# Kernel tuning notes

Measured on AMD Instinct MI355X. Metric: run time of the kernel, lower is better.

The kernel has to match this reference:

```python
import jax, jax.numpy as jnp
import numpy as np

T, B, DIM, D_INNER, N_STATE = 2048, 8, 1024, 2048, 64


def setup_inputs() -> dict:
    key = jax.random.key(0)
    ks = jax.random.split(key, 7)

    def w(k, shape, fan_in):
        return jax.random.normal(k, shape, jnp.float32) / np.float32(np.sqrt(fan_in))

    return {
        "x": jax.random.normal(ks[0], (T, B, DIM), jnp.float32),
        "W_in": w(ks[1], (D_INNER, DIM), DIM),      # in_proj (torch Linear weight layout)
        "W_k": w(ks[2], (N_STATE, D_INNER), D_INNER),
        "W_v": w(ks[3], (N_STATE, D_INNER), D_INNER),
        "W_q": w(ks[4], (N_STATE, D_INNER), D_INNER),
        "W_z": w(ks[5], (N_STATE, D_INNER), D_INNER),  # output-gate projection
        "W_out": w(ks[6], (DIM, N_STATE), N_STATE),  # out_proj
    }


def _forward(x, W_in, W_k, W_v, W_q, W_z, W_out):
    # x: [T, B, dim] -> h: [T, B, d_inner]
    h = jnp.einsum('tbd,id->tbi', x, W_in)
    # per-token cell projections: [T, B, n_state]
    k = jnp.einsum('tbi,ni->tbn', h, W_k)
    k = k / (jnp.linalg.norm(k, axis=-1, keepdims=True) + 1e-6)  # unit-norm key (stable delta rule)
    v = jnp.einsum('tbi,ni->tbn', h, W_v)
    q = jnp.einsum('tbi,ni->tbn', h, W_q)
    z = jnp.einsum('tbi,ni->tbn', h, W_z)

    S0 = jnp.zeros((x.shape[1], N_STATE, N_STATE), x.dtype)  # full-matrix state per batch

    def step(S, kvqz):
        kt, vt, qt, zt = kvqz                              # each [B, n_state]
        pred = jnp.einsum('bnm,bm->bn', S, kt)
        S = S + jnp.einsum('bn,bm->bnm', vt - pred, kt)    # delta-rule update
        y = jnp.tanh(jnp.einsum('bnm,bm->bn', S, qt)) * jax.nn.sigmoid(zt)  # tanh readout + output gate
        return S, y

    _, ys = jax.lax.scan(step, S0, (k, v, q, z))           # ys: [T, B, n_state]
    return jnp.einsum('tbn,dn->tbd', ys, W_out)            # out_proj -> [T, B, dim]


def reference(x, W_in, W_k, W_v, W_q, W_z, W_out):
    return _forward(x, W_in, W_k, W_v, W_q, W_z, W_out)
```

## Files before the change

kernel.cpp:

```cpp
#include <hip/hip_runtime.h>
#include <math.h>

#define TT   2048
#define BB   8
#define DIM_ 1024
#define DI_  2048
#define NS_  64
#define MR_  (TT * BB)
#define NCH  32
#define LD   68
#define KSPL 16
#define KCH  (DI_ / KSPL)
#define NGRP 8
#define GSZ  4
#define LDH2 40

typedef _Float16 half8 __attribute__((ext_vector_type(8)));
typedef _Float16 half4h __attribute__((ext_vector_type(4)));
typedef float floatx4 __attribute__((ext_vector_type(4)));

__device__ __forceinline__ float dot4(float4 a, float4 b) {
  return a.x * b.x + a.y * b.y + a.z * b.z + a.w * b.w;
}

__device__ __forceinline__ half8 cvt8(float4 lo, float4 hi) {
  half8 h = {(_Float16)lo.x, (_Float16)lo.y, (_Float16)lo.z, (_Float16)lo.w,
             (_Float16)hi.x, (_Float16)hi.y, (_Float16)hi.z, (_Float16)hi.w};
  return h;
}

__global__ __launch_bounds__(256) void cvt_f16_kernel(
    const float* __restrict__ in, _Float16* __restrict__ out, long n8) {
  long i = (long)blockIdx.x * 256 + threadIdx.x;
  const long stride = (long)gridDim.x * 256;
  for (; i < n8; i += stride) {
    const float4 lo = *(const float4*)&in[i * 8];
    const float4 hi = *(const float4*)&in[i * 8 + 4];
    *(half8*)&out[i * 8] = cvt8(lo, hi);
  }
}

__global__ __launch_bounds__(256) void gemm_h16(
    const _Float16* __restrict__ A, const _Float16* __restrict__ B,
    float* __restrict__ C, int M, int N, int K) {
  __shared__ __align__(16) _Float16 Ah[2][64 * LDH2];
  __shared__ __align__(16) _Float16 Bh[2][64 * LDH2];
  const int tid  = threadIdx.x;
  const int m0   = blockIdx.y * 64;
  const int n0   = blockIdx.x * 64;
  const int wave = tid >> 6, lane = tid & 63;
  const int wm   = (wave >> 1) * 32;
  const int wn   = (wave & 1) * 32;
  const int quad = lane >> 4, l16 = lane & 15;
  const int srow = tid >> 2;
  const int scol = (tid & 3) * 8;

  const _Float16* Ap = A + (size_t)(m0 + srow) * K + scol;
  const _Float16* Bp = B + (size_t)(n0 + srow) * K + scol;

  floatx4 acc[2][2];
#pragma unroll
  for (int i = 0; i < 2; ++i)
#pragma unroll
    for (int j = 0; j < 2; ++j) acc[i][j] = (floatx4)0.f;

  half8 ha, hb;
  ha = *(const half8*)(Ap);
  hb = *(const half8*)(Bp);
  *(half8*)&Ah[0][srow * LDH2 + scol] = ha;
  *(half8*)&Bh[0][srow * LDH2 + scol] = hb;
  __syncthreads();

  const int NK = K >> 5;
  for (int kt = 0; kt < NK; ++kt) {
    const int cur = kt & 1;
    if (kt + 1 < NK) {
      ha = *(const half8*)(Ap + (kt + 1) * 32);
      hb = *(const half8*)(Bp + (kt + 1) * 32);
    }
    half8 af[2], bf[2];
#pragma unroll
    for (int mt = 0; mt < 2; ++mt)
      af[mt] = *(const half8*)&Ah[cur][(wm + mt * 16 + l16) * LDH2 + quad * 8];
#pragma unroll
    for (int nt = 0; nt < 2; ++nt)
      bf[nt] = *(const half8*)&Bh[cur][(wn + nt * 16 + l16) * LDH2 + quad * 8];
#pragma unroll
    for (int mt = 0; mt < 2; ++mt)
#pragma unroll
      for (int nt = 0; nt < 2; ++nt)
        acc[mt][nt] = __builtin_amdgcn_mfma_f32_16x16x32_f16(
            af[mt], bf[nt], acc[mt][nt], 0, 0, 0);
    if (kt + 1 < NK) {
      const int nxt = cur ^ 1;
      *(half8*)&Ah[nxt][srow * LDH2 + scol] = ha;
      *(half8*)&Bh[nxt][srow * LDH2 + scol] = hb;
    }
    __syncthreads();
  }

#pragma unroll
  for (int mt = 0; mt < 2; ++mt) {
#pragma unroll
    for (int i = 0; i < 4; ++i) {
      const size_t r = (size_t)(m0 + wm + mt * 16 + quad * 4 + i) * N;
#pragma unroll
      for (int nt = 0; nt < 2; ++nt)
        C[r + n0 + wn + nt * 16 + l16] = acc[mt][nt][i];
    }
  }
}

__global__ __launch_bounds__(256) void fuse_gemm_kernel(
    const float* __restrict__ Wk, const float* __restrict__ Wv,
    const float* __restrict__ Wq, const float* __restrict__ Wz,
    const float* __restrict__ Win, float* __restrict__ Pg) {
  __shared__ __align__(16) float As[16][132];
  __shared__ __align__(16) float Bs[16][132];
  const int tid = threadIdx.x;
  const int n0  = blockIdx.x * 128;
  const int m0  = blockIdx.y * 128;
  const int kb  = blockIdx.z * KCH;
  const int lrow = tid >> 2;
  const int lk4  = (tid & 3) << 2;
  const int tm   = (tid & 15) << 2;
  const int tn   = (tid >> 4) << 2;
  const float* Wg[4] = {Wk, Wv, Wq, Wz};
  const int ra = m0 + lrow, rb = m0 + 64 + lrow;
  const float* arow0 = Wg[ra >> 6] + (size_t)(ra & 63) * DI_;
  const float* arow1 = Wg[rb >> 6] + (size_t)(rb & 63) * DI_;
  const int brow = tid >> 5;
  const int bcol = (tid & 31) << 2;

  float acc[8][8];
#pragma unroll
  for (int i = 0; i < 8; ++i)
#pragma unroll
    for (int j = 0; j < 8; ++j) acc[i][j] = 0.f;

  for (int k0 = 0; k0 < KCH; k0 += 16) {
    float4 av0 = *(const float4*)&arow0[kb + k0 + lk4];
    float4 av1 = *(const float4*)&arow1[kb + k0 + lk4];
    float4 bv0 = *(const float4*)&Win[(size_t)(kb + k0 + brow)     * DIM_ + n0 + bcol];
    float4 bv1 = *(const float4*)&Win[(size_t)(kb + k0 + 8 + brow) * DIM_ + n0 + bcol];
    __syncthreads();
    As[lk4 + 0][lrow] = av0.x; As[lk4 + 1][lrow] = av0.y;
    As[lk4 + 2][lrow] = av0.z; As[lk4 + 3][lrow] = av0.w;
    As[lk4 + 0][64 + lrow] = av1.x; As[lk4 + 1][64 + lrow] = av1.y;
    As[lk4 + 2][64 + lrow] = av1.z; As[lk4 + 3][64 + lrow] = av1.w;
    *(float4*)&Bs[brow][bcol]     = bv0;
    *(float4*)&Bs[brow + 8][bcol] = bv1;
    __syncthreads();
#pragma unroll
    for (int kk = 0; kk < 16; ++kk) {
      float4 a0 = *(const float4*)&As[kk][tm];
      float4 a1 = *(const float4*)&As[kk][tm + 64];
      float4 b0 = *(const float4*)&Bs[kk][tn];
      float4 b1 = *(const float4*)&Bs[kk][tn + 64];
      float ar[8] = {a0.x, a0.y, a0.z, a0.w, a1.x, a1.y, a1.z, a1.w};
      float br[8] = {b0.x, b0.y, b0.z, b0.w, b1.x, b1.y, b1.z, b1.w};
#pragma unroll
      for (int i = 0; i < 8; ++i)
#pragma unroll
        for (int j = 0; j < 8; ++j)
          acc[i][j] = fmaf(ar[i], br[j], acc[i][j]);
    }
  }
  float* P = Pg + (size_t)blockIdx.z * (256 * DIM_);
#pragma unroll
  for (int i = 0; i < 8; ++i) {
    int r = m0 + tm + (i & 3) + ((i >> 2) << 6);
    float4 c0 = make_float4(acc[i][0], acc[i][1], acc[i][2], acc[i][3]);
    float4 c1 = make_float4(acc[i][4], acc[i][5], acc[i][6], acc[i][7]);
    *(float4*)&P[(size_t)r * DIM_ + n0 + tn]      = c0;
    *(float4*)&P[(size_t)r * DIM_ + n0 + tn + 64] = c1;
  }
}

__global__ __launch_bounds__(256) void fuse_reduce_kernel(
    const float* __restrict__ Pg, _Float16* __restrict__ Wfh) {
  const size_t i = ((size_t)blockIdx.x * 256 + threadIdx.x) << 2;
  float4 s = *(const float4*)&Pg[i];
#pragma unroll
  for (int ks = 1; ks < KSPL; ++ks) {
    float4 p = *(const float4*)&Pg[(size_t)ks * (256 * DIM_) + i];
    s.x += p.x; s.y += p.y; s.z += p.z; s.w += p.w;
  }
  half4h h = {(_Float16)s.x, (_Float16)s.y, (_Float16)s.z, (_Float16)s.w};
  *(half4h*)&Wfh[i] = h;
}

__global__ __launch_bounds__(256) void norm_k_kernel(float* __restrict__ kvqz) {
  const int wid  = (blockIdx.x * 256 + threadIdx.x) >> 6;
  const int lane = threadIdx.x & 63;
  float x = kvqz[(size_t)wid * 256 + lane];
  float s = x * x;
  s += __shfl_xor(s, 1);  s += __shfl_xor(s, 2);  s += __shfl_xor(s, 4);
  s += __shfl_xor(s, 8);  s += __shfl_xor(s, 16); s += __shfl_xor(s, 32);
  kvqz[(size_t)wid * 256 + lane] = x / (sqrtf(s) + 1e-6f);
}

__global__ __launch_bounds__(256) void phase1_kernel(
    const float* __restrict__ kvqz, float* __restrict__ Tg,
    float* __restrict__ Mg, float* __restrict__ Bg) {
  __shared__ __align__(16) float Ks[64][LD];
  __shared__ __align__(16) float Vs[64][LD];
  __shared__ __align__(16) float As[64][LD];
  __shared__ __align__(16) float Tt[64][LD];
  const int cb = blockIdx.x;
  const int c  = cb >> 3, b = cb & 7;
  const int t  = threadIdx.x;

  {
    const int tau = t >> 2, m0 = (t & 3) << 4;
    const float* src = kvqz + (size_t)((c * 64 + tau) * BB + b) * 256;
#pragma unroll
    for (int u = 0; u < 4; ++u) {
      *(float4*)&Ks[tau][m0 + 4 * u] = *(const float4*)&src[m0 + 4 * u];
      *(float4*)&Vs[tau][m0 + 4 * u] = *(const float4*)&src[64 + m0 + 4 * u];
    }
  }
  __syncthreads();

  const int i0 = (t >> 4) << 2;
  const int j0 = (t & 15) << 2;

  {
    float acc[4][4];
#pragma unroll
    for (int i = 0; i < 4; ++i)
#pragma unroll
      for (int j = 0; j < 4; ++j) acc[i][j] = 0.f;
#pragma unroll 2
    for (int m4 = 0; m4 < 64; m4 += 4) {
      float4 ar[4], br[4];
#pragma unroll
      for (int i = 0; i < 4; ++i) ar[i] = *(const float4*)&Ks[i0 + i][m4];
#pragma unroll
      for (int j = 0; j < 4; ++j) br[j] = *(const float4*)&Ks[j0 + j][m4];
#pragma unroll
      for (int i = 0; i < 4; ++i)
#pragma unroll
        for (int j = 0; j < 4; ++j) acc[i][j] += dot4(ar[i], br[j]);
    }
#pragma unroll
    for (int i = 0; i < 4; ++i)
      *(float4*)&As[i0 + i][j0] =
          make_float4(acc[i][0], acc[i][1], acc[i][2], acc[i][3]);
  }
  __syncthreads();

  if (t < 64) {
    const int j = t;
    float tt[64];
    tt[0] = (j == 0) ? 1.f : 0.f;
#pragma unroll
    for (int i = 1; i < 64; ++i) {
      float p0 = 0.f, p1 = 0.f, p2 = 0.f, p3 = 0.f;
      const int nf = i >> 2;
#pragma unroll
      for (int s4 = 0; s4 < nf; ++s4) {
        float4 av = *(const float4*)&As[i][4 * s4];
        p0 = fmaf(av.x, tt[4 * s4 + 0], p0);
        p1 = fmaf(av.y, tt[4 * s4 + 1], p1);
        p2 = fmaf(av.z, tt[4 * s4 + 2], p2);
        p3 = fmaf(av.w, tt[4 * s4 + 3], p3);
      }
#pragma unroll
      for (int s = 4 * nf; s < i; ++s) p0 = fmaf(As[i][s], tt[s], p0);
      tt[i] = (i == j) ? 1.f : -((p0 + p1) + (p2 + p3));
    }
#pragma unroll
    for (int u = 0; u < 16; ++u)
      *(float4*)&Tt[j][4 * u] = make_float4(tt[4 * u + 0], tt[4 * u + 1],
                                            tt[4 * u + 2], tt[4 * u + 3]);
  }
  __syncthreads();

  {
    float accP[4][4], accV[4][4];
#pragma unroll
    for (int i = 0; i < 4; ++i)
#pragma unroll
      for (int j = 0; j < 4; ++j) { accP[i][j] = 0.f; accV[i][j] = 0.f; }
#pragma unroll 4
    for (int s = 0; s < 64; ++s) {
      float4 tv = *(const float4*)&Tt[s][i0];
      float4 kv = *(const float4*)&Ks[s][j0];
      float4 vv = *(const float4*)&Vs[s][j0];
      float ta[4] = {tv.x, tv.y, tv.z, tv.w};
      float ka[4] = {kv.x, kv.y, kv.z, kv.w};
      float va[4] = {vv.x, vv.y, vv.z, vv.w};
#pragma unroll
      for (int i = 0; i < 4; ++i)
#pragma unroll
        for (int j = 0; j < 4; ++j) {
          accP[i][j] = fmaf(ta[i], ka[j], accP[i][j]);
          accV[i][j] = fmaf(ta[i], va[j], accV[i][j]);
        }
    }
    __syncthreads();
#pragma unroll
    for (int i = 0; i < 4; ++i) {
      *(float4*)&As[i0 + i][j0] =
          make_float4(accP[i][0], accP[i][1], accP[i][2], accP[i][3]);
      *(float4*)&Vs[i0 + i][j0] =
          make_float4(accV[i][0], accV[i][1], accV[i][2], accV[i][3]);
    }
  }
  __syncthreads();

  {
    float accM[4][4], accB[4][4];
#pragma unroll
    for (int i = 0; i < 4; ++i)
#pragma unroll
      for (int j = 0; j < 4; ++j) { accM[i][j] = 0.f; accB[i][j] = 0.f; }
#pragma unroll 4
    for (int s = 0; s < 64; ++s) {
      float4 pv  = *(const float4*)&As[s][i0];
      float4 pvv = *(const float4*)&Vs[s][i0];
      float4 kv  = *(const float4*)&Ks[s][j0];
      float pa[4] = {pv.x, pv.y, pv.z, pv.w};
      float qa[4] = {pvv.x, pvv.y, pvv.z, pvv.w};
      float ka[4] = {kv.x, kv.y, kv.z, kv.w};
#pragma unroll
      for (int i = 0; i < 4; ++i)
#pragma unroll
        for (int j = 0; j < 4; ++j) {
          accM[i][j] = fmaf(pa[i], ka[j], accM[i][j]);
          accB[i][j] = fmaf(qa[i], ka[j], accB[i][j]);
        }
    }
    const size_t base = (size_t)cb * 4096;
#pragma unroll
    for (int i = 0; i < 4; ++i) {
      float m0v = ((i0 + i) == (j0 + 0)) ? 1.f : 0.f;
      float m1v = ((i0 + i) == (j0 + 1)) ? 1.f : 0.f;
      float m2v = ((i0 + i) == (j0 + 2)) ? 1.f : 0.f;
      float m3v = ((i0 + i) == (j0 + 3)) ? 1.f : 0.f;
      *(float4*)&Mg[base + (size_t)(i0 + i) * 64 + j0] =
          make_float4(m0v - accM[i][0], m1v - accM[i][1],
                      m2v - accM[i][2], m3v - accM[i][3]);
      *(float4*)&Bg[base + (size_t)(i0 + i) * 64 + j0] =
          make_float4(accB[i][0], accB[i][1], accB[i][2], accB[i][3]);
    }
    const int fr = t >> 2, fc = (t & 3) << 4;
#pragma unroll
    for (int u = 0; u < 4; ++u)
      *(float4*)&Tg[base + (size_t)fr * 64 + fc + 4 * u] =
          *(const float4*)&Tt[fr][fc + 4 * u];
  }
}

__global__ __launch_bounds__(64, 1) void p2a_kernel(
    const float* __restrict__ Mg, const float* __restrict__ Bg,
    float* __restrict__ Mcum, float* __restrict__ Sall,
    float* __restrict__ BGfin) {
  __shared__ __align__(16) float Srow[2][4 * LD];
  const int bid  = blockIdx.x;
  const int g    = bid >> 8;
  const int b    = (bid >> 5) & 7;
  const int w    = bid & 31;
  const int lane = threadIdx.x;
  const int rr   = lane >> 4;
  const int jc   = lane & 15;
  const bool isB = (w >= 16);
  const int n    = ((w & 15) << 2) + rr;

  float4 cs;
  if (isB) cs = make_float4(0.f, 0.f, 0.f, 0.f);
  else
    cs = make_float4((jc * 4 + 0) == n ? 1.f : 0.f,
                     (jc * 4 + 1) == n ? 1.f : 0.f,
                     (jc * 4 + 2) == n ? 1.f : 0.f,
                     (jc * 4 + 3) == n ? 1.f : 0.f);

  for (int l = 0; l < GSZ; ++l) {
    const int c   = g * GSZ + l;
    const int cur = l & 1;
    const size_t cbase = ((size_t)c * BB + b) * 4096;
    if (isB) *(float4*)&Sall[cbase + (size_t)n * 64 + jc * 4] = cs;
    else if (l > 0) *(float4*)&Mcum[cbase + (size_t)n * 64 + jc * 4] = cs;
    *(float4*)&Srow[cur][rr * LD + jc * 4] = cs;
    float4 bv = make_float4(0.f, 0.f, 0.f, 0.f);
    if (isB) bv = *(const float4*)&Bg[cbase + (size_t)n * 64 + jc * 4];

    const float* Mrow = Mg + cbase + jc * 4;
    float4 acc = make_float4(0.f, 0.f, 0.f, 0.f);
#pragma unroll
    for (int u = 0; u < 16; ++u) {
      float4 sv = *(const float4*)&Srow[cur][rr * LD + u * 4];
      float4 m0 = *(const float4*)&Mrow[(4 * u + 0) * 64];
      float4 m1 = *(const float4*)&Mrow[(4 * u + 1) * 64];
      float4 m2 = *(const float4*)&Mrow[(4 * u + 2) * 64];
      float4 m3 = *(const float4*)&Mrow[(4 * u + 3) * 64];
      acc.x = fmaf(sv.x, m0.x, acc.x); acc.y = fmaf(sv.x, m0.y, acc.y);
      acc.z = fmaf(sv.x, m0.z, acc.z); acc.w = fmaf(sv.x, m0.w, acc.w);
      acc.x = fmaf(sv.y, m1.x, acc.x); acc.y = fmaf(sv.y, m1.y, acc.y);
      acc.z = fmaf(sv.y, m1.z, acc.z); acc.w = fmaf(sv.y, m1.w, acc.w);
      acc.x = fmaf(sv.z, m2.x, acc.x); acc.y = fmaf(sv.z, m2.y, acc.y);
      acc.z = fmaf(sv.z, m2.z, acc.z); acc.w = fmaf(sv.z, m2.w, acc.w);
      acc.x = fmaf(sv.w, m3.x, acc.x); acc.y = fmaf(sv.w, m3.y, acc.y);
      acc.z = fmaf(sv.w, m3.z, acc.z); acc.w = fmaf(sv.w, m3.w, acc.w);
    }
    cs = make_float4(acc.x + bv.x, acc.y + bv.y, acc.z + bv.z, acc.w + bv.w);
  }
  if (isB)
    *(float4*)&BGfin[((size_t)g * BB + b) * 4096 + (size_t)n * 64 + jc * 4] = cs;
  else
    *(float4*)&Mcum[((size_t)(g * GSZ) * BB + b) * 4096 + (size_t)n * 64 + jc * 4] = cs;
}

__global__ __launch_bounds__(64, 1) void p2b_kernel(
    const float* __restrict__ Mcum, const float* __restrict__ BGfin,
    float* __restrict__ Sall) {
  __shared__ __align__(16) float Srow[2][4 * LD];
  const int bid  = blockIdx.x;
  const int b    = bid >> 4;
  const int w    = bid & 15;
  const int lane = threadIdx.x;
  const int rr   = lane >> 4;
  const int jc   = lane & 15;
  const int n    = w * 4 + rr;

  float4 cs = make_float4(0.f, 0.f, 0.f, 0.f);

  for (int g2 = 0; g2 < NGRP - 1; ++g2) {
    const int cur = g2 & 1;
    *(float4*)&Srow[cur][rr * LD + jc * 4] = cs;
    float4 bv = *(const float4*)&BGfin[((size_t)g2 * BB + b) * 4096 +
                                       (size_t)n * 64 + jc * 4];
    const float* Mrow =
        Mcum + ((size_t)(g2 * GSZ) * BB + b) * 4096 + jc * 4;
    float4 acc = make_float4(0.f, 0.f, 0.f, 0.f);
#pragma unroll
    for (int u = 0; u < 16; ++u) {
      float4 sv = *(const float4*)&Srow[cur][rr * LD + u * 4];
      float4 m0 = *(const float4*)&Mrow[(4 * u + 0) * 64];
      float4 m1 = *(const float4*)&Mrow[(4 * u + 1) * 64];
      float4 m2 = *(const float4*)&Mrow[(4 * u + 2) * 64];
      float4 m3 = *(const float4*)&Mrow[(4 * u + 3) * 64];
      acc.x = fmaf(sv.x, m0.x, acc.x); acc.y = fmaf(sv.x, m0.y, acc.y);
      acc.z = fmaf(sv.x, m0.z, acc.z); acc.w = fmaf(sv.x, m0.w, acc.w);
      acc.x = fmaf(sv.y, m1.x, acc.x); acc.y = fmaf(sv.y, m1.y, acc.y);
      acc.z = fmaf(sv.y, m1.z, acc.z); acc.w = fmaf(sv.y, m1.w, acc.w);
      acc.x = fmaf(sv.z, m2.x, acc.x); acc.y = fmaf(sv.z, m2.y, acc.y);
      acc.z = fmaf(sv.z, m2.z, acc.z); acc.w = fmaf(sv.z, m2.w, acc.w);
      acc.x = fmaf(sv.w, m3.x, acc.x); acc.y = fmaf(sv.w, m3.y, acc.y);
      acc.z = fmaf(sv.w, m3.z, acc.z); acc.w = fmaf(sv.w, m3.w, acc.w);
    }
    cs = make_float4(acc.x + bv.x, acc.y + bv.y, acc.z + bv.z, acc.w + bv.w);
    *(float4*)&Sall[((size_t)((g2 + 1) * GSZ) * BB + b) * 4096 +
                    (size_t)n * 64 + jc * 4] = cs;
  }
}

__global__ __launch_bounds__(256) void p2c_kernel(
    const float* __restrict__ Mcum, float* __restrict__ Sall) {
  __shared__ __align__(16) float SgT[64][LD];
  __shared__ __align__(16) float Mc[64][LD];
  const int idx = blockIdx.x;
  const int b   = idx & 7;
  const int q   = idx >> 3;
  const int g   = 1 + q / (GSZ - 1);
  const int l   = 1 + q % (GSZ - 1);
  const int c   = g * GSZ + l;
  const int t   = threadIdx.x;
  const size_t cbase = ((size_t)c * BB + b) * 4096;
  const size_t gbase = ((size_t)(g * GSZ) * BB + b) * 4096;
  {
    const int tau = t & 63, c0 = (t >> 6) << 4;
    const float* sgp = Sall + gbase + (size_t)tau * 64 + c0;
    const float* mcp = Mcum + cbase + (size_t)tau * 64 + c0;
#pragma unroll
    for (int u = 0; u < 4; ++u) {
      float4 sv = *(const float4*)&sgp[4 * u];
      SgT[c0 + 4 * u + 0][tau] = sv.x;
      SgT[c0 + 4 * u + 1][tau] = sv.y;
      SgT[c0 + 4 * u + 2][tau] = sv.z;
      SgT[c0 + 4 * u + 3][tau] = sv.w;
      *(float4*)&Mc[tau][c0 + 4 * u] = *(const float4*)&mcp[4 * u];
    }
  }
  __syncthreads();
  const int i0 = (t >> 4) << 2;
  const int j0 = (t & 15) << 2;
  float acc[4][4];
#pragma unroll
  for (int i = 0; i < 4; ++i)
#pragma unroll
    for (int j = 0; j < 4; ++j) acc[i][j] = 0.f;
  for (int m = 0; m < 64; ++m) {
    float4 tv = *(const float4*)&SgT[m][i0];
    float4 kv = *(const float4*)&Mc[m][j0];
    float ta[4] = {tv.x, tv.y, tv.z, tv.w};
    float ka[4] = {kv.x, kv.y, kv.z, kv.w};
#pragma unroll
    for (int i = 0; i < 4; ++i)
#pragma unroll
      for (int j = 0; j < 4; ++j) acc[i][j] = fmaf(ta[i], ka[j], acc[i][j]);
  }
  float* dst = Sall + cbase;
#pragma unroll
  for (int i = 0; i < 4; ++i) {
    float4 d = *(float4*)&dst[(size_t)(i0 + i) * 64 + j0];
    d.x += acc[i][0]; d.y += acc[i][1];
    d.z += acc[i][2]; d.w += acc[i][3];
    *(float4*)&dst[(size_t)(i0 + i) * 64 + j0] = d;
  }
}

__global__ __launch_bounds__(256) void phase3_kernel(
    const float* __restrict__ kvqz, const float* __restrict__ Tg,
    const float* __restrict__ Sall, _Float16* __restrict__ ys) {
  __shared__ __align__(16) float Ks[64][LD];
  __shared__ __align__(16) float Qs[64][LD];
  __shared__ __align__(16) float S0s[64][LD];
  __shared__ __align__(16) float Gts[64][LD];
  const int cb = blockIdx.x;
  const int c  = cb >> 3, b = cb & 7;
  const int t  = threadIdx.x;
  const size_t base = (size_t)cb * 4096;

  {
    const int tau = t >> 2, m0 = (t & 3) << 4;
    const float* src = kvqz + (size_t)((c * 64 + tau) * BB + b) * 256;
#pragma unroll
    for (int u = 0; u < 4; ++u) {
      *(float4*)&Ks[tau][m0 + 4 * u]  = *(const float4*)&src[m0 + 4 * u];
      *(float4*)&Qs[tau][m0 + 4 * u]  = *(const float4*)&src[128 + m0 + 4 * u];
      *(float4*)&S0s[tau][m0 + 4 * u] = *(const float4*)&Sall[base + (size_t)tau * 64 + m0 + 4 * u];
    }
  }
  __syncthreads();

  const int i0 = (t >> 4) << 2;
  const int j0 = (t & 15) << 2;

  {
    float acc[4][4];
#pragma unroll
    for (int i = 0; i < 4; ++i)
#pragma unroll
      for (int j = 0; j < 4; ++j) acc[i][j] = 0.f;
#pragma unroll 2
    for (int m4 = 0; m4 < 64; m4 += 4) {
      float4 kr[4], qr[4];
#pragma unroll
      for (int i = 0; i < 4; ++i) kr[i] = *(const float4*)&Ks[i0 + i][m4];
#pragma unroll
      for (int j = 0; j < 4; ++j) qr[j] = *(const float4*)&Qs[j0 + j][m4];
#pragma unroll
      for (int i = 0; i < 4; ++i)
#pragma unroll
        for (int j = 0; j < 4; ++j) acc[i][j] += dot4(kr[i], qr[j]);
    }
#pragma unroll
    for (int i = 0; i < 4; ++i)
      *(float4*)&Gts[i0 + i][j0] =
          make_float4(acc[i][0], acc[i][1], acc[i][2], acc[i][3]);
  }

  {
    float acc[4][4];
#pragma unroll
    for (int i = 0; i < 4; ++i) {
      const float* vrow = kvqz + (size_t)((c * 64 + i0 + i) * BB + b) * 256 + 64;
      float4 vv = *(const float4*)&vrow[j0];
      acc[i][0] = vv.x; acc[i][1] = vv.y; acc[i][2] = vv.z; acc[i][3] = vv.w;
    }
#pragma unroll 2
    for (int m4 = 0; m4 < 64; m4 += 4) {
      float4 kr[4], sr[4];
#pragma unroll
      for (int i = 0; i < 4; ++i) kr[i] = *(const float4*)&Ks[i0 + i][m4];
#pragma unroll
      for (int j = 0; j < 4; ++j) sr[j] = *(const float4*)&S0s[j0 + j][m4];
#pragma unroll
      for (int i = 0; i < 4; ++i)
#pragma unroll
        for (int j = 0; j < 4; ++j) acc[i][j] -= dot4(kr[i], sr[j]);
    }
    __syncthreads();
#pragma unroll
    for (int i = 0; i < 4; ++i)
      *(float4*)&Ks[i0 + i][j0] =
          make_float4(acc[i][0], acc[i][1], acc[i][2], acc[i][3]);
  }
  __syncthreads();

  float4 zv[4];
  {
#pragma unroll
    for (int i = 0; i < 4; ++i) {
      const float* zrow = kvqz + (size_t)((c * 64 + i0 + i) * BB + b) * 256 + 192;
      zv[i] = *(const float4*)&zrow[j0];
    }
    float acc[4][4];
#pragma unroll
    for (int i = 0; i < 4; ++i)
#pragma unroll
      for (int j = 0; j < 4; ++j) acc[i][j] = 0.f;
    const float* Tp = Tg + base + i0;
#pragma unroll 4
    for (int s = 0; s < 64; ++s) {
      float4 tv = *(const float4*)&Tp[(size_t)s * 64];
      float4 wv = *(const float4*)&Ks[s][j0];
      float ta[4] = {tv.x, tv.y, tv.z, tv.w};
      float wa[4] = {wv.x, wv.y, wv.z, wv.w};
#pragma unroll
      for (int i = 0; i < 4; ++i)
#pragma unroll
        for (int j = 0; j < 4; ++j) acc[i][j] = fmaf(ta[i], wa[j], acc[i][j]);
    }
    __syncthreads();
#pragma unroll
    for (int i = 0; i < 4; ++i)
      *(float4*)&Ks[i0 + i][j0] =
          make_float4(acc[i][0], acc[i][1], acc[i][2], acc[i][3]);
  }
  __syncthreads();

  {
    float acc[4][4];
#pragma unroll
    for (int i = 0; i < 4; ++i)
#pragma unroll
      for (int j = 0; j < 4; ++j) acc[i][j] = 0.f;
#pragma unroll 2
    for (int m4 = 0; m4 < 64; m4 += 4) {
      float4 qr[4], sr[4];
#pragma unroll
      for (int i = 0; i < 4; ++i) qr[i] = *(const float4*)&Qs[i0 + i][m4];
#pragma unroll
      for (int j = 0; j < 4; ++j) sr[j] = *(const float4*)&S0s[j0 + j][m4];
#pragma unroll
      for (int i = 0; i < 4; ++i)
#pragma unroll
        for (int j = 0; j < 4; ++j) acc[i][j] += dot4(qr[i], sr[j]);
    }
#pragma unroll 4
    for (int s = 0; s < 64; ++s) {
      float4 gv = *(const float4*)&Gts[s][i0];
      float4 uv = *(const float4*)&Ks[s][j0];
      float ga[4] = {gv.x, gv.y, gv.z, gv.w};
      float ua[4] = {uv.x, uv.y, uv.z, uv.w};
#pragma unroll
      for (int i = 0; i < 4; ++i) {
        float gi = (s <= i0 + i) ? ga[i] : 0.f;
#pragma unroll
        for (int j = 0; j < 4; ++j) acc[i][j] = fmaf(gi, ua[j], acc[i][j]);
      }
    }
#pragma unroll
    for (int i = 0; i < 4; ++i) {
      float za[4] = {zv[i].x, zv[i].y, zv[i].z, zv[i].w};
      _Float16 oh[4];
#pragma unroll
      for (int j = 0; j < 4; ++j) {
        float e2 = __expf(2.f * acc[i][j]);
        float th = 1.f - 2.f / (e2 + 1.f);
        float sg = 1.f / (1.f + __expf(-za[j]));
        oh[j] = (_Float16)(th * sg);
      }
      half4h o4 = {oh[0], oh[1], oh[2], oh[3]};
      *(half4h*)&ys[(size_t)((c * 64 + i0 + i) * BB + b) * 64 + j0] = o4;
    }
  }
}

extern "C" void kernel_launch(void* const* d_in, const int* in_sizes, int n_in,
                              void* d_out, int out_size, void* d_ws, size_t ws_size,
                              hipStream_t stream) {
  const float* x    = (const float*)d_in[0];
  const float* Win  = (const float*)d_in[1];
  const float* Wk   = (const float*)d_in[2];
  const float* Wv   = (const float*)d_in[3];
  const float* Wq   = (const float*)d_in[4];
  const float* Wz   = (const float*)d_in[5];
  const float* Wout = (const float*)d_in[6];
  float* out = (float*)d_out;

  char* ws = (char*)d_ws;
  _Float16* Wfh  = (_Float16*)(ws);
  float* BGfin   = (float*)(ws);
  _Float16* Woh  = (_Float16*)(ws);
  float* kvqz    = (float*)(ws + (1u  << 20));
  _Float16* ysh  = (_Float16*)(ws + (17u << 20));
  float* Mcum    = (float*)(ws + (17u << 20));
  float* Tg      = (float*)(ws + (21u << 20));
  float* Mg      = (float*)(ws + (25u << 20));
  float* Bg      = (float*)(ws + (29u << 20));
  float* Sall    = (float*)(ws + (33u << 20));
  float* Pg      = (float*)(ws + (21u << 20));
  _Float16* xh   = (_Float16*)(ws + (21u << 20));

  fuse_gemm_kernel<<<dim3(DIM_ / 128, 2, KSPL), 256, 0, stream>>>(Wk, Wv, Wq, Wz, Win, Pg);
  fuse_reduce_kernel<<<(256 * DIM_ / 4) / 256, 256, 0, stream>>>(Pg, Wfh);

  if (ws_size >= (53ull << 20)) {
    cvt_f16_kernel<<<2048, 256, 0, stream>>>(x, xh, (long)MR_ * DIM_ / 8);
    gemm_h16<<<dim3(256 / 64, MR_ / 64), 256, 0, stream>>>(xh, Wfh, kvqz, MR_, 256, DIM_);
  } else {
    const long half_rows = MR_ / 2;
    for (int h = 0; h < 2; ++h) {
      const float* xs = x + (size_t)h * half_rows * DIM_;
      float* cs = kvqz + (size_t)h * half_rows * 256;
      cvt_f16_kernel<<<2048, 256, 0, stream>>>(xs, xh, half_rows * DIM_ / 8);
      gemm_h16<<<dim3(256 / 64, (int)(half_rows / 64)), 256, 0, stream>>>(
          xh, Wfh, cs, (int)half_rows, 256, DIM_);
    }
  }

  norm_k_kernel<<<MR_ / 4, 256, 0, stream>>>(kvqz);
  phase1_kernel<<<NCH * BB, 256, 0, stream>>>(kvqz, Tg, Mg, Bg);
  p2a_kernel<<<NGRP * BB * 32, 64, 0, stream>>>(Mg, Bg, Mcum, Sall, BGfin);
  p2b_kernel<<<16 * BB, 64, 0, stream>>>(Mcum, BGfin, Sall);
  p2c_kernel<<<(NGRP - 1) * (GSZ - 1) * BB, 256, 0, stream>>>(Mcum, Sall);
  cvt_f16_kernel<<<32, 256, 0, stream>>>(Wout, Woh, (long)(DIM_ * NS_ / 8));
  phase3_kernel<<<NCH * BB, 256, 0, stream>>>(kvqz, Tg, Sall, ysh);
  gemm_h16<<<dim3(DIM_ / 64, MR_ / 64), 256, 0, stream>>>(ysh, Woh, out, MR_, DIM_, NS_);
}
```

Baseline: 284.7 us.

## Use fp16 MFMA for weight-fusion GEMM and fold key normalization into phase kernels

Replaces the fp32 scalar-FMA weight-fusion GEMM (16-way split-K plus reduce) with fp16 packing and transposition of the weights, then an MFMA split-K GEMM with 4 splits. The standalone norm_k kernel is dropped and the key normalization is computed inline when phase1 and phase3 load K into LDS. The Gram-matrix B-operand reads are also reindexed to a strided column pattern, likely to reduce LDS bank conflicts. This removes a kernel launch and a full pass over kvqz, at the cost of extra pack and transpose kernels, fp16 rounding of the weights before the product, and normalization done twice.

```diff
diff --git a/kernel.cpp b/kernel.cpp
--- a/kernel.cpp
+++ b/kernel.cpp
@@ -9,11 +9,10 @@
 #define MR_  (TT * BB)
 #define NCH  32
 #define LD   68
-#define KSPL 16
-#define KCH  (DI_ / KSPL)
 #define NGRP 8
 #define GSZ  4
 #define LDH2 40
+#define FKS  4
 
 typedef _Float16 half8 __attribute__((ext_vector_type(8)));
 typedef _Float16 half4h __attribute__((ext_vector_type(4)));
@@ -37,6 +36,50 @@
     const float4 lo = *(const float4*)&in[i * 8];
     const float4 hi = *(const float4*)&in[i * 8 + 4];
     *(half8*)&out[i * 8] = cvt8(lo, hi);
+  }
+}
+
+__global__ __launch_bounds__(256) void pack_wg_kernel(
+    const float* __restrict__ Wk, const float* __restrict__ Wv,
+    const float* __restrict__ Wq, const float* __restrict__ Wz,
+    _Float16* __restrict__ Wgh) {
+  const float* Wg[4] = {Wk, Wv, Wq, Wz};
+  const long g = (long)blockIdx.x * 256 + threadIdx.x;
+  const int row = (int)(g >> 8);
+  const int k   = (int)((g & 255) << 3);
+  const float* src = Wg[row >> 6] + (size_t)(row & 63) * DI_ + k;
+  const float4 lo = *(const float4*)&src[0];
+  const float4 hi = *(const float4*)&src[4];
+  *(half8*)&Wgh[(size_t)row * DI_ + k] = cvt8(lo, hi);
+}
+
+__global__ __launch_bounds__(256) void transpose_win_kernel(
+    const float* __restrict__ Win, _Float16* __restrict__ WinTh) {
+  __shared__ float T[64][65];
+  const int t  = threadIdx.x;
+  const int c0 = blockIdx.x * 64;
+  const int r0 = blockIdx.y * 64;
+  {
+    const int tr = t >> 2, tc = (t & 3) * 16;
+#pragma unroll
+    for (int u = 0; u < 4; ++u) {
+      float4 v = *(const float4*)&Win[(size_t)(r0 + tr) * DIM_ + c0 + tc + 4 * u];
+      T[tr][tc + 4 * u + 0] = v.x;
+      T[tr][tc + 4 * u + 1] = v.y;
+      T[tr][tc + 4 * u + 2] = v.z;
+      T[tr][tc + 4 * u + 3] = v.w;
+    }
+  }
+  __syncthreads();
+  {
+    const int oc = t >> 2;
+    const int orr = (t & 3) * 16;
+    _Float16 h[16];
+#pragma unroll
+    for (int u = 0; u < 16; ++u) h[u] = (_Float16)T[orr + u][oc];
+    _Float16* dst = WinTh + (size_t)(c0 + oc) * DI_ + r0 + orr;
+    *(half8*)&dst[0] = *(half8*)&h[0];
+    *(half8*)&dst[8] = *(half8*)&h[8];
   }
 }
 
@@ -111,93 +154,90 @@
   }
 }
 
-__global__ __launch_bounds__(256) void fuse_gemm_kernel(
-    const float* __restrict__ Wk, const float* __restrict__ Wv,
-    const float* __restrict__ Wq, const float* __restrict__ Wz,
-    const float* __restrict__ Win, float* __restrict__ Pg) {
-  __shared__ __align__(16) float As[16][132];
-  __shared__ __align__(16) float Bs[16][132];
-  const int tid = threadIdx.x;
-  const int n0  = blockIdx.x * 128;
-  const int m0  = blockIdx.y * 128;
-  const int kb  = blockIdx.z * KCH;
-  const int lrow = tid >> 2;
-  const int lk4  = (tid & 3) << 2;
-  const int tm   = (tid & 15) << 2;
-  const int tn   = (tid >> 4) << 2;
-  const float* Wg[4] = {Wk, Wv, Wq, Wz};
-  const int ra = m0 + lrow, rb = m0 + 64 + lrow;
-  const float* arow0 = Wg[ra >> 6] + (size_t)(ra & 63) * DI_;
-  const float* arow1 = Wg[rb >> 6] + (size_t)(rb & 63) * DI_;
-  const int brow = tid >> 5;
-  const int bcol = (tid & 31) << 2;
-
-  float acc[8][8];
-#pragma unroll
-  for (int i = 0; i < 8; ++i)
-#pragma unroll
-    for (int j = 0; j < 8; ++j) acc[i][j] = 0.f;
-
-  for (int k0 = 0; k0 < KCH; k0 += 16) {
-    float4 av0 = *(const float4*)&arow0[kb + k0 + lk4];
-    float4 av1 = *(const float4*)&arow1[kb + k0 + lk4];
-    float4 bv0 = *(const float4*)&Win[(size_t)(kb + k0 + brow)     * DIM_ + n0 + bcol];
-    float4 bv1 = *(const float4*)&Win[(size_t)(kb + k0 + 8 + brow) * DIM_ + n0 + bcol];
+__global__ __launch_bounds__(256) void gemm_h16_splitk(
+    const _Float16* __restrict__ A, const _Float16* __restrict__ B,
+    float* __restrict__ Cp, int M, int N, int K, int kchunk) {
+  __shared__ __align__(16) _Float16 Ah[2][64 * LDH2];
+  __shared__ __align__(16) _Float16 Bh[2][64 * LDH2];
+  const int tid  = threadIdx.x;
+  const int m0   = blockIdx.y * 64;
+  const int n0   = blockIdx.x * 64;
+  const int kb   = blockIdx.z * kchunk;
+  const int wave = tid >> 6, lane = tid & 63;
+  const int wm   = (wave >> 1) * 32;
+  const int wn   = (wave & 1) * 32;
+  const int quad = lane >> 4, l16 = lane & 15;
+  const int srow = tid >> 2;
+  const int scol = (tid & 3) * 8;
+
+  const _Float16* Ap = A + (size_t)(m0 + srow) * K + kb + scol;
+  const _Float16* Bp = B + (size_t)(n0 + srow) * K + kb + scol;
+  float* C = Cp + (size_t)blockIdx.z * M * N;
+
+  floatx4 acc[2][2];
+#pragma unroll
+  for (int i = 0; i < 2; ++i)
+#pragma unroll
+    for (int j = 0; j < 2; ++j) acc[i][j] = (floatx4)0.f;
+
+  half8 ha, hb;
+  ha = *(const half8*)(Ap);
+  hb = *(const half8*)(Bp);
+  *(half8*)&Ah[0][srow * LDH2 + scol] = ha;
+  *(half8*)&Bh[0][srow * LDH2 + scol] = hb;
+  __syncthreads();
+
+  const int NK = kchunk >> 5;
+  for (int kt = 0; kt < NK; ++kt) {
+    const int cur = kt & 1;
+    if (kt + 1 < NK) {
+      ha = *(const half8*)(Ap + (kt + 1) * 32);
+      hb = *(const half8*)(Bp + (kt + 1) * 32);
+    }
+    half8 af[2], bf[2];
+#pragma unroll
+    for (int mt = 0; mt < 2; ++mt)
+      af[mt] = *(const half8*)&Ah[cur][(wm + mt * 16 + l16) * LDH2 + quad * 8];
+#pragma unroll
+    for (int nt = 0; nt < 2; ++nt)
+      bf[nt] = *(const half8*)&Bh[cur][(wn + nt * 16 + l16) * LDH2 + quad * 8];
+#pragma unroll
+    for (int mt = 0; mt < 2; ++mt)
+#pragma unroll
+      for (int nt = 0; nt < 2; ++nt)
+        acc[mt][nt] = __builtin_amdgcn_mfma_f32_16x16x32_f16(
+            af[mt], bf[nt], acc[mt][nt], 0, 0, 0);
+    if (kt + 1 < NK) {
+      const int nxt = cur ^ 1;
+      *(half8*)&Ah[nxt][srow * LDH2 + scol] = ha;
+      *(half8*)&Bh[nxt][srow * LDH2 + scol] = hb;
+    }
     __syncthreads();
-    As[lk4 + 0][lrow] = av0.x; As[lk4 + 1][lrow] = av0.y;
-    As[lk4 + 2][lrow] = av0.z; As[lk4 + 3][lrow] = av0.w;
-    As[lk4 + 0][64 + lrow] = av1.x; As[lk4 + 1][64 + lrow] = av1.y;
-    As[lk4 + 2][64 + lrow] = av1.z; As[lk4 + 3][64 + lrow] = av1.w;
-    *(float4*)&Bs[brow][bcol]     = bv0;
-    *(float4*)&Bs[brow + 8][bcol] = bv1;
-    __syncthreads();
-#pragma unroll
-    for (int kk = 0; kk < 16; ++kk) {
-      float4 a0 = *(const float4*)&As[kk][tm];
-      float4 a1 = *(const float4*)&As[kk][tm + 64];
-      float4 b0 = *(const float4*)&Bs[kk][tn];
-      float4 b1 = *(const float4*)&Bs[kk][tn + 64];
-      float ar[8] = {a0.x, a0.y, a0.z, a0.w, a1.x, a1.y, a1.z, a1.w};
-      float br[8] = {b0.x, b0.y, b0.z, b0.w, b1.x, b1.y, b1.z, b1.w};
-#pragma unroll
-      for (int i = 0; i < 8; ++i)
-#pragma unroll
-        for (int j = 0; j < 8; ++j)
-          acc[i][j] = fmaf(ar[i], br[j], acc[i][j]);
-    }
-  }
-  float* P = Pg + (size_t)blockIdx.z * (256 * DIM_);
-#pragma unroll
-  for (int i = 0; i < 8; ++i) {
-    int r = m0 + tm + (i & 3) + ((i >> 2) << 6);
-    float4 c0 = make_float4(acc[i][0], acc[i][1], acc[i][2], acc[i][3]);
-    float4 c1 = make_float4(acc[i][4], acc[i][5], acc[i][6], acc[i][7]);
-    *(float4*)&P[(size_t)r * DIM_ + n0 + tn]      = c0;
-    *(float4*)&P[(size_t)r * DIM_ + n0 + tn + 64] = c1;
-  }
-}
-
-__global__ __launch_bounds__(256) void fuse_reduce_kernel(
-    const float* __restrict__ Pg, _Float16* __restrict__ Wfh) {
+  }
+
+#pragma unroll
+  for (int mt = 0; mt < 2; ++mt) {
+#pragma unroll
+    for (int i = 0; i < 4; ++i) {
+      const size_t r = (size_t)(m0 + wm + mt * 16 + quad * 4 + i) * N;
+#pragma unroll
+      for (int nt = 0; nt < 2; ++nt)
+        C[r + n0 + wn + nt * 16 + l16] = acc[mt][nt][i];
+    }
+  }
+}
+
+__global__ __launch_bounds__(256) void fuse_reduce4_kernel(
+    const float* __restrict__ Pg4, _Float16* __restrict__ Wfh) {
   const size_t i = ((size_t)blockIdx.x * 256 + threadIdx.x) << 2;
-  float4 s = *(const float4*)&Pg[i];
-#pragma unroll
-  for (int ks = 1; ks < KSPL; ++ks) {
-    float4 p = *(const float4*)&Pg[(size_t)ks * (256 * DIM_) + i];
+  float4 s = *(const float4*)&Pg4[i];
+#pragma unroll
+  for (int z = 1; z < FKS; ++z) {
+    float4 p = *(const float4*)&Pg4[(size_t)z * (256 * DIM_) + i];
     s.x += p.x; s.y += p.y; s.z += p.z; s.w += p.w;
   }
   half4h h = {(_Float16)s.x, (_Float16)s.y, (_Float16)s.z, (_Float16)s.w};
   *(half4h*)&Wfh[i] = h;
-}
-
-__global__ __launch_bounds__(256) void norm_k_kernel(float* __restrict__ kvqz) {
-  const int wid  = (blockIdx.x * 256 + threadIdx.x) >> 6;
-  const int lane = threadIdx.x & 63;
-  float x = kvqz[(size_t)wid * 256 + lane];
-  float s = x * x;
-  s += __shfl_xor(s, 1);  s += __shfl_xor(s, 2);  s += __shfl_xor(s, 4);
-  s += __shfl_xor(s, 8);  s += __shfl_xor(s, 16); s += __shfl_xor(s, 32);
-  kvqz[(size_t)wid * 256 + lane] = x / (sqrtf(s) + 1e-6f);
 }
 
 __global__ __launch_bounds__(256) void phase1_kernel(
@@ -212,18 +252,30 @@
   const int t  = threadIdx.x;
 
   {
-    const int tau = t >> 2, m0 = (t & 3) << 4;
+    const int tau = t >> 2, m0q = (t & 3) << 4;
     const float* src = kvqz + (size_t)((c * 64 + tau) * BB + b) * 256;
+    float4 kv[4];
+    float ss = 0.f;
 #pragma unroll
     for (int u = 0; u < 4; ++u) {
-      *(float4*)&Ks[tau][m0 + 4 * u] = *(const float4*)&src[m0 + 4 * u];
-      *(float4*)&Vs[tau][m0 + 4 * u] = *(const float4*)&src[64 + m0 + 4 * u];
+      kv[u] = *(const float4*)&src[m0q + 4 * u];
+      ss += dot4(kv[u], kv[u]);
+      *(float4*)&Vs[tau][m0q + 4 * u] = *(const float4*)&src[64 + m0q + 4 * u];
+    }
+    ss += __shfl_xor(ss, 1);
+    ss += __shfl_xor(ss, 2);
+    const float sc = 1.f / (sqrtf(ss) + 1e-6f);
+#pragma unroll
+    for (int u = 0; u < 4; ++u) {
+      kv[u].x *= sc; kv[u].y *= sc; kv[u].z *= sc; kv[u].w *= sc;
+      *(float4*)&Ks[tau][m0q + 4 * u] = kv[u];
     }
   }
   __syncthreads();
 
   const int i0 = (t >> 4) << 2;
   const int j0 = (t & 15) << 2;
+  const int jc = t & 15;
 
   {
     float acc[4][4];
@@ -237,7 +289,7 @@
 #pragma unroll
       for (int i = 0; i < 4; ++i) ar[i] = *(const float4*)&Ks[i0 + i][m4];
 #pragma unroll
-      for (int j = 0; j < 4; ++j) br[j] = *(const float4*)&Ks[j0 + j][m4];
+      for (int j = 0; j < 4; ++j) br[j] = *(const float4*)&Ks[jc + 16 * j][m4];
 #pragma unroll
       for (int i = 0; i < 4; ++i)
 #pragma unroll
@@ -245,8 +297,8 @@
     }
 #pragma unroll
     for (int i = 0; i < 4; ++i)
-      *(float4*)&As[i0 + i][j0] =
-          make_float4(acc[i][0], acc[i][1], acc[i][2], acc[i][3]);
+#pragma unroll
+      for (int j = 0; j < 4; ++j) As[i0 + i][jc + 16 * j] = acc[i][j];
   }
   __syncthreads();
 
@@ -524,19 +576,31 @@
   const size_t base = (size_t)cb * 4096;
 
   {
-    const int tau = t >> 2, m0 = (t & 3) << 4;
+    const int tau = t >> 2, m0q = (t & 3) << 4;
     const float* src = kvqz + (size_t)((c * 64 + tau) * BB + b) * 256;
+    float4 kv[4];
+    float ss = 0.f;
 #pragma unroll
     for (int u = 0; u < 4; ++u) {
-      *(float4*)&Ks[tau][m0 + 4 * u]  = *(const float4*)&src[m0 + 4 * u];
-      *(float4*)&Qs[tau][m0 + 4 * u]  = *(const float4*)&src[128 + m0 + 4 * u];
-      *(float4*)&S0s[tau][m0 + 4 * u] = *(const float4*)&Sall[base + (size_t)tau * 64 + m0 + 4 * u];
+      kv[u] = *(const float4*)&src[m0q + 4 * u];
+      ss += dot4(kv[u], kv[u]);
+      *(float4*)&Qs[tau][m0q + 4 * u]  = *(const float4*)&src[128 + m0q + 4 * u];
+      *(float4*)&S0s[tau][m0q + 4 * u] = *(const float4*)&Sall[base + (size_t)tau * 64 + m0q + 4 * u];
+    }
+    ss += __shfl_xor(ss, 1);
+    ss += __shfl_xor(ss, 2);
+    const float sc = 1.f / (sqrtf(ss) + 1e-6f);
+#pragma unroll
+    for (int u = 0; u < 4; ++u) {
+      kv[u].x *= sc; kv[u].y *= sc; kv[u].z *= sc; kv[u].w *= sc;
+      *(float4*)&Ks[tau][m0q + 4 * u] = kv[u];
     }
   }
   __syncthreads();
 
   const int i0 = (t >> 4) << 2;
   const int j0 = (t & 15) << 2;
+  const int jc = t & 15;
 
   {
     float acc[4][4];
@@ -550,7 +614,7 @@
 #pragma unroll
       for (int i = 0; i < 4; ++i) kr[i] = *(const float4*)&Ks[i0 + i][m4];
 #pragma unroll
-      for (int j = 0; j < 4; ++j) qr[j] = *(const float4*)&Qs[j0 + j][m4];
+      for (int j = 0; j < 4; ++j) qr[j] = *(const float4*)&Qs[jc + 16 * j][m4];
 #pragma unroll
       for (int i = 0; i < 4; ++i)
 #pragma unroll
@@ -558,8 +622,8 @@
     }
 #pragma unroll
     for (int i = 0; i < 4; ++i)
-      *(float4*)&Gts[i0 + i][j0] =
-          make_float4(acc[i][0], acc[i][1], acc[i][2], acc[i][3]);
+#pragma unroll
+      for (int j = 0; j < 4; ++j) Gts[i0 + i][jc + 16 * j] = acc[i][j];
   }
 
   {
@@ -689,15 +753,20 @@
   float* kvqz    = (float*)(ws + (1u  << 20));
   _Float16* ysh  = (_Float16*)(ws + (17u << 20));
   float* Mcum    = (float*)(ws + (17u << 20));
+  _Float16* Wgh  = (_Float16*)(ws + (21u << 20));
+  _Float16* WinTh= (_Float16*)(ws + (22u << 20));
+  float* Pg4     = (float*)(ws + (26u << 20));
   float* Tg      = (float*)(ws + (21u << 20));
   float* Mg      = (float*)(ws + (25u << 20));
   float* Bg      = (float*)(ws + (29u << 20));
   float* Sall    = (float*)(ws + (33u << 20));
-  float* Pg      = (float*)(ws + (21u << 20));
   _Float16* xh   = (_Float16*)(ws + (21u << 20));
 
-  fuse_gemm_kernel<<<dim3(DIM_ / 128, 2, KSPL), 256, 0, stream>>>(Wk, Wv, Wq, Wz, Win, Pg);
-  fuse_reduce_kernel<<<(256 * DIM_ / 4) / 256, 256, 0, stream>>>(Pg, Wfh);
+  pack_wg_kernel<<<256, 256, 0, stream>>>(Wk, Wv, Wq, Wz, Wgh);
+  transpose_win_kernel<<<dim3(DIM_ / 64, DI_ / 64), 256, 0, stream>>>(Win, WinTh);
+  gemm_h16_splitk<<<dim3(DIM_ / 64, 256 / 64, FKS), 256, 0, stream>>>(
+      Wgh, WinTh, Pg4, 256, DIM_, DI_, DI_ / FKS);
+  fuse_reduce4_kernel<<<(256 * DIM_ / 4) / 256, 256, 0, stream>>>(Pg4, Wfh);
 
   if (ws_size >= (53ull << 20)) {
     cvt_f16_kernel<<<2048, 256, 0, stream>>>(x, xh, (long)MR_ * DIM_ / 8);
@@ -713,7 +782,6 @@
     }
   }
 
-  norm_k_kernel<<<MR_ / 4, 256, 0, stream>>>(kvqz);
   phase1_kernel<<<NCH * BB, 256, 0, stream>>>(kvqz, Tg, Mg, Bg);
   p2a_kernel<<<NGRP * BB * 32, 64, 0, stream>>>(Mg, Bg, Mcum, Sall, BGfin);
   p2b_kernel<<<16 * BB, 64, 0, stream>>>(Mcum, BGfin, Sall);
```

After: 269.3 us. 1.06x faster.
